# Optimization experiments

Measured on AMD Instinct MI355X. Metric: run time of the kernel, lower is better.

The kernel has to match this reference:

```python
import jax, jax.numpy as jnp
import numpy as np

NUM_CLASSES = 21
NUM_BOXES = 8732
BATCH = 128


def setup_inputs() -> dict:
    key = jax.random.key(0)
    k1, k2, k3, k4 = jax.random.split(key, 4)
    return {
        "loc_preds": jax.random.normal(k1, (BATCH, NUM_BOXES, 4), dtype=jnp.float32),
        "loc_targets": jax.random.normal(k2, (BATCH, NUM_BOXES, 4), dtype=jnp.float32),
        "conf_preds": jax.random.normal(k3, (BATCH, NUM_BOXES, NUM_CLASSES), dtype=jnp.float32),
        "label_targets": jax.random.randint(k4, (BATCH, NUM_BOXES), 0, NUM_CLASSES, dtype=jnp.int64),
    }


def reference(loc_preds, loc_targets, conf_preds, label_targets):
    n, num_boxes, _ = conf_preds.shape
    pos = label_targets > 0                                   # [n, B] matched boxes
    num_matched = jnp.sum(pos).astype(conf_preds.dtype)

    # --- localization loss: smooth L1 (beta=1) summed over positive boxes ---
    diff = loc_preds - loc_targets
    ad = jnp.abs(diff)
    sl1 = jnp.where(ad < 1.0, 0.5 * diff * diff, ad - 0.5)    # [n, B, 4]
    loc_loss = jnp.sum(jnp.where(pos[:, :, None], sl1, 0.0))

    # --- per-box CE for mining (original uses a single global max for logsumexp) ---
    x_max = jax.lax.stop_gradient(jnp.max(conf_preds))
    lse = jnp.log(jnp.sum(jnp.exp(conf_preds - x_max), axis=-1)) + x_max   # [n, B]
    gold = jnp.take_along_axis(conf_preds, label_targets[..., None], axis=-1)[..., 0]
    mining_loss = jnp.where(pos, -1.0, lse - gold)            # pos boxes forced lowest

    # --- hard negative mining: double argsort -> rank of each box's loss ---
    idx = jnp.argsort(-mining_loss, axis=1)                   # descending sort indices
    rank = jnp.argsort(idx, axis=1)                           # rank of each box
    num_pos = jnp.sum(pos.astype(jnp.int32), axis=1)          # [n]
    num_neg = jnp.minimum(3 * num_pos, num_boxes - 1)         # [n]
    neg = rank < num_neg[:, None]
    sel = pos | neg                                           # [n, B]

    # --- confidence loss: standard CE over selected boxes (F.cross_entropy) ---
    logp = jax.nn.log_softmax(conf_preds, axis=-1)
    ce = -jnp.take_along_axis(logp, label_targets[..., None], axis=-1)[..., 0]
    conf_loss = jnp.sum(jnp.where(sel, ce, 0.0))

    denom = jnp.maximum(num_matched, 1.0)
    return (loc_loss + conf_loss) / denom
```

## Files before the change

### kernel.cpp

```cpp
#include <hip/hip_runtime.h>

#define NB 8732
#define NC 21
#define BATCH 128
#define GPT 2183
#define GXB 9

__device__ inline float wred_f(float v) {
#pragma unroll
    for (int o = 32; o > 0; o >>= 1) v += __shfl_down(v, o, 64);
    return v;
}
__device__ inline int wred_i(int v) {
#pragma unroll
    for (int o = 32; o > 0; o >>= 1) v += __shfl_down(v, o, 64);
    return v;
}

#define QV(f) (((f) & 3) == 0 ? q[(f) >> 2].x : ((f) & 3) == 1 ? q[(f) >> 2].y \
             : ((f) & 3) == 2 ? q[(f) >> 2].z : q[(f) >> 2].w)

__global__ void __launch_bounds__(256)
kA(const float* __restrict__ locp, const float* __restrict__ loct,
   const float* __restrict__ conf, const int* __restrict__ lab,
   float* __restrict__ row_ce, float* __restrict__ row_pce,
   int* __restrict__ row_np, float* __restrict__ loc_acc,
   int* __restrict__ nm_acc) {
    const int r = blockIdx.y;
    const int g = blockIdx.x * 256 + threadIdx.x;

    float ceS = 0.f, pceS = 0.f, llS = 0.f;
    int npS = 0;

    if (g < GPT) {
        const size_t box0 = (size_t)r * NB + (size_t)g * 4;
        const float4* __restrict__ src = (const float4*)(conf + box0 * NC);
        float4 q[21];
#pragma unroll
        for (int k = 0; k < 21; k++) q[k] = src[k];

        const int4 lb4 = *(const int4*)(lab + box0);
        const int lbv[4] = {lb4.x, lb4.y, lb4.z, lb4.w};

        const float4* __restrict__ lpp = (const float4*)(locp + box0 * 4);
        const float4* __restrict__ ltp = (const float4*)(loct + box0 * 4);

#pragma unroll
        for (int b = 0; b < 4; b++) {
            const int l = lbv[b];
            float m = QV(b * 21);
#pragma unroll
            for (int j = 1; j < 21; j++) m = fmaxf(m, QV(b * 21 + j));
            float s = 0.f, gold = 0.f;
#pragma unroll
            for (int j = 0; j < 21; j++) {
                const float cv = QV(b * 21 + j);
                s += __expf(cv - m);
                gold = (j == l) ? cv : gold;
            }
            const float ce = m + __logf(s) - gold;
            ceS += ce;
            if (l > 0) {
                npS++;
                pceS += ce;
                const float4 lp = lpp[b];
                const float4 lt = ltp[b];
                float d, ad;
                d = lp.x - lt.x; ad = fabsf(d); llS += (ad < 1.f) ? 0.5f * d * d : ad - 0.5f;
                d = lp.y - lt.y; ad = fabsf(d); llS += (ad < 1.f) ? 0.5f * d * d : ad - 0.5f;
                d = lp.z - lt.z; ad = fabsf(d); llS += (ad < 1.f) ? 0.5f * d * d : ad - 0.5f;
                d = lp.w - lt.w; ad = fabsf(d); llS += (ad < 1.f) ? 0.5f * d * d : ad - 0.5f;
            }
        }
    }

    __shared__ float sr[3][4];
    __shared__ int si[4];
    float v0 = wred_f(ceS), v1 = wred_f(pceS), v2 = wred_f(llS);
    int v3 = wred_i(npS);
    const int w = threadIdx.x >> 6, ln = threadIdx.x & 63;
    if (ln == 0) { sr[0][w] = v0; sr[1][w] = v1; sr[2][w] = v2; si[w] = v3; }
    __syncthreads();
    if (threadIdx.x == 0) {
        float A = 0, B = 0, C = 0; int D = 0;
#pragma unroll
        for (int k = 0; k < 4; k++) { A += sr[0][k]; B += sr[1][k]; C += sr[2][k]; D += si[k]; }
        atomicAdd(&row_ce[r], A);
        atomicAdd(&row_pce[r], B);
        atomicAdd(loc_acc, C);
        atomicAdd(&row_np[r], D);
        atomicAdd(nm_acc, D);
    }
}

__device__ inline float ce_for_box0(const float* __restrict__ cp) {
    float c[NC];
#pragma unroll
    for (int j = 0; j < NC; j++) c[j] = cp[j];
    float m = c[0];
#pragma unroll
    for (int j = 1; j < NC; j++) m = fmaxf(m, c[j]);
    float s = 0.f;
#pragma unroll
    for (int j = 0; j < NC; j++) s += __expf(c[j] - m);
    return m + __logf(s) - c[0];
}

__global__ void __launch_bounds__(256)
kB(const float* __restrict__ conf, const int* __restrict__ lab,
   const float* __restrict__ row_ce, const float* __restrict__ row_pce,
   const int* __restrict__ row_np, float* __restrict__ conf_acc,
   float* __restrict__ loc_acc, int* __restrict__ nm_acc,
   int* __restrict__ done, float* __restrict__ out) {
    const int r = blockIdx.x;
    const int np = row_np[r];
    const int K = min(3 * np, NB - 1);
    const int nneg = NB - np;

    float rowval = 0.f;
    if (K >= nneg) {
        rowval = row_ce[r];
    } else if (K <= 0) {
        rowval = row_pce[r];
    } else {
        __shared__ unsigned key[NB];
        __shared__ unsigned hist[256];
        __shared__ unsigned sb[2];
        for (int i = threadIdx.x; i < NB; i += 256) {
            const long box = (long)r * NB + i;
            unsigned k = 0u;
            if (lab[box] == 0) {
                float ce = ce_for_box0(conf + box * (long)NC);
                k = __float_as_uint(fmaxf(ce, 0.f));
            }
            key[i] = k;
        }
        __syncthreads();
        unsigned prefix = 0;
        int Kr = K;
        for (int round = 3; round >= 0; --round) {
            const int sh = round * 8;
            const unsigned pmask = (round == 3) ? 0u : (0xFFFFFFFFu << (8 * (round + 1)));
            for (int b = threadIdx.x; b < 256; b += 256) hist[b] = 0;
            __syncthreads();
            for (int i = threadIdx.x; i < NB; i += 256) {
                const unsigned k = key[i];
                if ((k & pmask) == prefix) atomicAdd(&hist[(k >> sh) & 255u], 1u);
            }
            __syncthreads();
            if (threadIdx.x == 0) {
                unsigned cum = 0; int b = 255;
                for (; b > 0; --b) {
                    const unsigned h = hist[b];
                    if (cum + h >= (unsigned)Kr) break;
                    cum += h;
                }
                sb[0] = cum; sb[1] = (unsigned)b;
            }
            __syncthreads();
            Kr -= (int)sb[0];
            prefix |= (sb[1] << sh);
            __syncthreads();
        }
        float local = 0.f;
        for (int i = threadIdx.x; i < NB; i += 256) {
            const unsigned k = key[i];
            if (k > prefix) local += __uint_as_float(k);
        }
        __shared__ float sred[4];
        float v = wred_f(local);
        const int w = threadIdx.x >> 6, ln = threadIdx.x & 63;
        if (ln == 0) sred[w] = v;
        __syncthreads();
        rowval = row_pce[r] + sred[0] + sred[1] + sred[2] + sred[3]
               + (float)Kr * __uint_as_float(prefix);
    }

    if (threadIdx.x == 0) {
        atomicAdd(conf_acc, rowval);
        __threadfence();
        const int old = atomicAdd(done, 1);
        if (old == BATCH - 1) {
            const float cf = atomicAdd(conf_acc, 0.f);
            const float lc = atomicAdd(loc_acc, 0.f);
            const int nm = atomicAdd(nm_acc, 0);
            out[0] = (lc + cf) / fmaxf((float)nm, 1.f);
        }
    }
}

extern "C" void kernel_launch(void* const* d_in, const int* in_sizes, int n_in,
                              void* d_out, int out_size, void* d_ws, size_t ws_size,
                              hipStream_t stream) {
    const float* locp = (const float*)d_in[0];
    const float* loct = (const float*)d_in[1];
    const float* conf = (const float*)d_in[2];
    const int* lab = (const int*)d_in[3];
    float* out = (float*)d_out;

    float* loc_acc = (float*)d_ws;
    float* conf_acc = loc_acc + 1;
    int* nm_acc = (int*)d_ws + 2;
    int* done = (int*)d_ws + 3;
    float* row_ce = (float*)d_ws + 16;
    float* row_pce = row_ce + BATCH;
    int* row_np = (int*)(row_pce + BATCH);

    hipMemsetAsync(d_ws, 0, 4096, stream);

    hipLaunchKernelGGL(kA, dim3(GXB, BATCH), dim3(256), 0, stream,
                       locp, loct, conf, lab, row_ce, row_pce, row_np, loc_acc, nm_acc);
    hipLaunchKernelGGL(kB, dim3(BATCH), dim3(256), 0, stream,
                       conf, lab, row_ce, row_pce, row_np, conf_acc, loc_acc, nm_acc, done, out);
}
```

Before: 192.9 us.

## Stage conf logits through per-wave LDS for coalesced loads, one box per thread

Kernel A now gives one box to each thread instead of four, with each wave handling 64 consecutive boxes. Each wave loads the 64×21 logits with fully coalesced strided reads into a per-wave shared-memory buffer, then every thread reads its own box's 21 values back from LDS. This replaces the per-thread 21×float4 strided vector loads, which were poorly coalesced and heavy on registers. It also launches about four times as many blocks for more parallelism, at the cost of 21 KB of LDS per block and extra LDS traffic.

```diff
diff --git a/kernel.cpp b/kernel.cpp
--- a/kernel.cpp
+++ b/kernel.cpp
@@ -3,8 +3,7 @@
 #define NB 8732
 #define NC 21
 #define BATCH 128
-#define GPT 2183
-#define GXB 9
+#define BX 35
 
 __device__ inline float wred_f(float v) {
 #pragma unroll
@@ -16,9 +15,6 @@
     for (int o = 32; o > 0; o >>= 1) v += __shfl_down(v, o, 64);
     return v;
 }
-
-#define QV(f) (((f) & 3) == 0 ? q[(f) >> 2].x : ((f) & 3) == 1 ? q[(f) >> 2].y \
-             : ((f) & 3) == 2 ? q[(f) >> 2].z : q[(f) >> 2].w)
 
 __global__ void __launch_bounds__(256)
 kA(const float* __restrict__ locp, const float* __restrict__ loct,
@@ -26,45 +22,64 @@
    float* __restrict__ row_ce, float* __restrict__ row_pce,
    int* __restrict__ row_np, float* __restrict__ loc_acc,
    int* __restrict__ nm_acc) {
+    __shared__ float xb[4][1344];
     const int r = blockIdx.y;
-    const int g = blockIdx.x * 256 + threadIdx.x;
+    const int w = threadIdx.x >> 6;
+    const int ln = threadIdx.x & 63;
+    const int box0 = blockIdx.x * 256 + w * 64;
 
     float ceS = 0.f, pceS = 0.f, llS = 0.f;
     int npS = 0;
 
-    if (g < GPT) {
-        const size_t box0 = (size_t)r * NB + (size_t)g * 4;
-        const float4* __restrict__ src = (const float4*)(conf + box0 * NC);
-        float4 q[21];
-#pragma unroll
-        for (int k = 0; k < 21; k++) q[k] = src[k];
-
-        const int4 lb4 = *(const int4*)(lab + box0);
-        const int lbv[4] = {lb4.x, lb4.y, lb4.z, lb4.w};
-
-        const float4* __restrict__ lpp = (const float4*)(locp + box0 * 4);
-        const float4* __restrict__ ltp = (const float4*)(loct + box0 * 4);
-
-#pragma unroll
-        for (int b = 0; b < 4; b++) {
-            const int l = lbv[b];
-            float m = QV(b * 21);
-#pragma unroll
-            for (int j = 1; j < 21; j++) m = fmaxf(m, QV(b * 21 + j));
-            float s = 0.f, gold = 0.f;
+    if (box0 < NB) {
+        const int cnt = min(64, NB - box0);
+        const size_t rowbase = (size_t)r * NB;
+        const float* __restrict__ src = conf + (rowbase + box0) * (size_t)NC;
+
+        int l = 0;
+        float4 lp = {0.f, 0.f, 0.f, 0.f}, lt = {0.f, 0.f, 0.f, 0.f};
+        if (ln < cnt) {
+            const size_t box = rowbase + box0 + ln;
+            l = lab[box];
+            lp = *(const float4*)(locp + box * 4);
+            lt = *(const float4*)(loct + box * 4);
+        }
+
+        if (cnt == 64) {
+            float v[21];
+#pragma unroll
+            for (int j = 0; j < 21; j++) v[j] = src[64 * j + ln];
+#pragma unroll
+            for (int j = 0; j < 21; j++) xb[w][64 * j + ln] = v[j];
+        } else {
+            const int nflat = cnt * NC;
 #pragma unroll
             for (int j = 0; j < 21; j++) {
-                const float cv = QV(b * 21 + j);
-                s += __expf(cv - m);
-                gold = (j == l) ? cv : gold;
-            }
+                const int idx = 64 * j + ln;
+                if (idx < nflat) xb[w][idx] = src[idx];
+            }
+        }
+        asm volatile("s_waitcnt lgkmcnt(0)" ::: "memory");
+
+        if (ln < cnt) {
+            float c[21];
+            const float* bp = &xb[w][21 * ln];
+#pragma unroll
+            for (int j = 0; j < 21; j++) c[j] = bp[j];
+            float m = c[0];
+#pragma unroll
+            for (int j = 1; j < 21; j++) m = fmaxf(m, c[j]);
+            float s = 0.f;
+#pragma unroll
+            for (int j = 0; j < 21; j++) s += __expf(c[j] - m);
+            float gold = c[0];
+#pragma unroll
+            for (int j = 1; j < 21; j++) gold = (j == l) ? c[j] : gold;
             const float ce = m + __logf(s) - gold;
-            ceS += ce;
+            ceS = ce;
             if (l > 0) {
-                npS++;
-                pceS += ce;
-                const float4 lp = lpp[b];
-                const float4 lt = ltp[b];
+                npS = 1;
+                pceS = ce;
                 float d, ad;
                 d = lp.x - lt.x; ad = fabsf(d); llS += (ad < 1.f) ? 0.5f * d * d : ad - 0.5f;
                 d = lp.y - lt.y; ad = fabsf(d); llS += (ad < 1.f) ? 0.5f * d * d : ad - 0.5f;
@@ -78,7 +93,6 @@
     __shared__ int si[4];
     float v0 = wred_f(ceS), v1 = wred_f(pceS), v2 = wred_f(llS);
     int v3 = wred_i(npS);
-    const int w = threadIdx.x >> 6, ln = threadIdx.x & 63;
     if (ln == 0) { sr[0][w] = v0; sr[1][w] = v1; sr[2][w] = v2; si[w] = v3; }
     __syncthreads();
     if (threadIdx.x == 0) {
@@ -208,7 +222,7 @@
 
     hipMemsetAsync(d_ws, 0, 4096, stream);
 
-    hipLaunchKernelGGL(kA, dim3(GXB, BATCH), dim3(256), 0, stream,
+    hipLaunchKernelGGL(kA, dim3(BX, BATCH), dim3(256), 0, stream,
                        locp, loct, conf, lab, row_ce, row_pce, row_np, loc_acc, nm_acc);
     hipLaunchKernelGGL(kB, dim3(BATCH), dim3(256), 0, stream,
                        conf, lab, row_ce, row_pce, row_np, conf_acc, loc_acc, nm_acc, done, out);
```

Result: slower. 251.7 us (+30.5%).
